# Kernel tuning notes

Hardware: AMD Instinct MI355X
Metric: run time of the kernel (lower is better)

## Reference

```python
import jax, jax.numpy as jnp
import numpy as np

N_NODES = 16   # number of per-node submodules in the DAG (topological order)
D = 2048       # per-node feature width (d_model)
B = 4096       # batch size of the in_graph tensor


def setup_inputs() -> dict:
    key = jax.random.key(0)
    kx, kw, kb = jax.random.split(key, 3)
    x = jax.random.normal(kx, (B, D), dtype=jnp.float32)
    # Per-node dense weights, scaled ~1/sqrt(D) so tanh stays in its linear-ish range
    W = jax.random.normal(kw, (N_NODES, D, D), dtype=jnp.float32) / np.float32(np.sqrt(D))
    b = jax.random.normal(kb, (N_NODES, D), dtype=jnp.float32) * np.float32(0.01)
    return {"x": x, "W": W, "b": b}


def reference(x, W, b):
    # Faithful DAG executor: iterate nodes in topological order; the address
    # book maps node i -> predecessor outputs {i-1, i-2} (node 0 reads x).
    # Each node module computes y = tanh(sum(inputs) @ W_i + b_i).
    # Loop is over the fixed structural node set (not a data dimension).
    outs = []
    for i in range(N_NODES):
        if i == 0:
            inp = x
        elif i == 1:
            inp = outs[0]
        else:
            inp = outs[i - 1] + outs[i - 2]  # address-book fan-in (sum of predecessors)
        y = jnp.tanh(inp @ W[i] + b[i])  # [B, D]
        outs.append(y)
    # _eval_forward returns the single terminal output of the DAG
    return outs[-1]
```

## Files before the change

kernel.cpp:

```cpp
#include <hip/hip_runtime.h>
#include <cstdint>
#include <cstddef>

#define NN 16
#define DD 2048
#define BB 4096

#define TM 128
#define TN 128
#define BK 64

typedef _Float16 half8 __attribute__((ext_vector_type(8)));
typedef _Float16 half4 __attribute__((ext_vector_type(4)));
typedef float f32x4 __attribute__((ext_vector_type(4)));

__device__ __forceinline__ float fast_tanh(float x) {
  float ax = __builtin_fabsf(x);
  float e = __expf(-2.0f * ax);
  float t = (1.0f - e) / (1.0f + e);
  return x < 0.0f ? -t : t;
}

__global__ __launch_bounds__(256) void wconv_kernel(const float* __restrict__ W,
                                                    _Float16* __restrict__ Wh) {
  __shared__ _Float16 tile[64][80];
  const int i = blockIdx.z;
  const int k0 = blockIdx.y * 64;
  const int n0 = blockIdx.x * 64;
  const float* Wi = W + (size_t)i * DD * DD;
  _Float16* Whi = Wh + (size_t)i * DD * DD;
  const int t = threadIdx.x;
  const int cr = t >> 4;
  const int cc = (t & 15) * 4;
#pragma unroll
  for (int p = 0; p < 4; ++p) {
    int r = p * 16 + cr;
    float4 v = *(const float4*)(Wi + (size_t)(k0 + r) * DD + n0 + cc);
    tile[cc + 0][r] = (_Float16)v.x;
    tile[cc + 1][r] = (_Float16)v.y;
    tile[cc + 2][r] = (_Float16)v.z;
    tile[cc + 3][r] = (_Float16)v.w;
  }
  __syncthreads();
  const int wr = t >> 3;
  const int wc = (t & 7) * 8;
#pragma unroll
  for (int p = 0; p < 2; ++p) {
    int n = p * 32 + wr;
    half8 v = *(const half8*)&tile[n][wc];
    *(half8*)(Whi + (size_t)(n0 + n) * DD + k0 + wc) = v;
  }
}

__global__ __launch_bounds__(256) void xconv_kernel(const float* __restrict__ x,
                                                    _Float16* __restrict__ s0) {
  size_t idx = (size_t)(blockIdx.x * 256 + threadIdx.x) * 4;
  float4 v = *(const float4*)(x + idx);
  half4 o;
  o.x = (_Float16)v.x; o.y = (_Float16)v.y; o.z = (_Float16)v.z; o.w = (_Float16)v.w;
  *(half4*)(s0 + idx) = o;
}

__global__ __launch_bounds__(256, 2) void node_gemm(
    const _Float16* __restrict__ S,
    const _Float16* __restrict__ Wt,
    const float* __restrict__ bias,
    _Float16* __restrict__ Y,
    const _Float16* __restrict__ Yprev,
    _Float16* __restrict__ Snext,
    float* __restrict__ Ofinal)
{
  __shared__ _Float16 smem[4 * TM * BK];

  const int t = threadIdx.x;
  const int lane = t & 63;
  const int wave = t >> 6;
  const int bid = blockIdx.x;
  const int n0 = (bid & 15) * TN;
  const int m0 = (bid >> 4) * TM;
  const int wm = (wave & 1) * 64;
  const int wn = (wave >> 1) * 64;
  const int lrow = lane & 15;
  const int lq = lane >> 4;

  f32x4 acc[4][4];
#pragma unroll
  for (int i = 0; i < 4; ++i)
#pragma unroll
    for (int j = 0; j < 4; ++j) acc[i][j] = (f32x4)0.0f;

  const int srow = t >> 3;
  const int ska = ((t & 7) ^ (srow & 7)) * 8;
  const _Float16* ag = S + (size_t)(m0 + srow) * DD + ska;
  const _Float16* bg = Wt + (size_t)(n0 + srow) * DD + ska;

  auto stage = [&](int p, int k0) {
    const _Float16* a = ag + k0;
    const _Float16* b = bg + k0;
    _Float16* al = smem + p * (TM * BK) + t * 8;
    _Float16* bl = smem + 2 * (TM * BK) + p * (TN * BK) + t * 8;
#pragma unroll
    for (int r = 0; r < 4; ++r) {
      __builtin_amdgcn_global_load_lds(
          (const __attribute__((address_space(1))) void*)(a + (size_t)(r * 32) * DD),
          (__attribute__((address_space(3))) void*)(al + r * 2048), 16, 0, 0);
      __builtin_amdgcn_global_load_lds(
          (const __attribute__((address_space(1))) void*)(b + (size_t)(r * 32) * DD),
          (__attribute__((address_space(3))) void*)(bl + r * 2048), 16, 0, 0);
    }
  };

  stage(0, 0);

  for (int i = 0; i < DD / BK; ++i) {
    __syncthreads();
    if (i < DD / BK - 1) stage((i + 1) & 1, (i + 1) * BK);
    const _Float16* Ap = smem + (i & 1) * (TM * BK);
    const _Float16* Bp = smem + 2 * (TM * BK) + (i & 1) * (TN * BK);
#pragma unroll
    for (int ks = 0; ks < BK; ks += 32) {
      const int cx = (((ks >> 3) + lq) ^ (lrow & 7)) * 8;
      half8 a[4], b[4];
#pragma unroll
      for (int mt = 0; mt < 4; ++mt)
        a[mt] = *(const half8*)(Ap + (wm + mt * 16 + lrow) * BK + cx);
#pragma unroll
      for (int nt = 0; nt < 4; ++nt)
        b[nt] = *(const half8*)(Bp + (wn + nt * 16 + lrow) * BK + cx);
#pragma unroll
      for (int mt = 0; mt < 4; ++mt)
#pragma unroll
        for (int nt = 0; nt < 4; ++nt)
          acc[mt][nt] =
              __builtin_amdgcn_mfma_f32_16x16x32_f16(a[mt], b[nt], acc[mt][nt], 0, 0, 0);
    }
  }

  __syncthreads();
  _Float16* CT = smem;
  float bv[4];
#pragma unroll
  for (int nt = 0; nt < 4; ++nt) bv[nt] = bias[n0 + wn + nt * 16 + lrow];
#pragma unroll
  for (int mt = 0; mt < 4; ++mt)
#pragma unroll
    for (int nt = 0; nt < 4; ++nt)
#pragma unroll
      for (int r = 0; r < 4; ++r) {
        int row = wm + mt * 16 + lq * 4 + r;
        int col = wn + nt * 16 + lrow;
        CT[row * TN + col] = (_Float16)fast_tanh(acc[mt][nt][r] + bv[nt]);
      }
  __syncthreads();

#pragma unroll
  for (int pp = 0; pp < 8; ++pp) {
    int idx = pp * 2048 + t * 8;
    int row = idx >> 7;
    int col = idx & 127;
    size_t off = (size_t)(m0 + row) * DD + n0 + col;
    half8 y = *(const half8*)&CT[idx];
    if (Ofinal) {
      float4 f0 = {(float)y[0], (float)y[1], (float)y[2], (float)y[3]};
      float4 f1 = {(float)y[4], (float)y[5], (float)y[6], (float)y[7]};
      *(float4*)(Ofinal + off) = f0;
      *(float4*)(Ofinal + off + 4) = f1;
    } else {
      *(half8*)(Y + off) = y;
      half8 s = y;
      if (Yprev) s = s + *(const half8*)(Yprev + off);
      *(half8*)(Snext + off) = s;
    }
  }
}

extern "C" void kernel_launch(void* const* d_in, const int* in_sizes, int n_in,
                              void* d_out, int out_size, void* d_ws, size_t ws_size,
                              hipStream_t stream) {
  const float* x = (const float*)d_in[0];
  const float* W = (const float*)d_in[1];
  const float* b = (const float*)d_in[2];
  float* out = (float*)d_out;
  char* ws = (char*)d_ws;

  _Float16* Wh = (_Float16*)ws;
  size_t wbytes = (size_t)NN * DD * DD * sizeof(_Float16);
  _Float16* S0 = (_Float16*)(ws + wbytes);
  _Float16* S1 = S0 + (size_t)BB * DD;
  _Float16* Y0 = S1 + (size_t)BB * DD;
  _Float16* Y1 = Y0 + (size_t)BB * DD;

  wconv_kernel<<<dim3(DD / 64, DD / 64, NN), dim3(256), 0, stream>>>(W, Wh);
  xconv_kernel<<<dim3((BB * DD) / 1024), dim3(256), 0, stream>>>(x, S0);

  _Float16* Sb[2] = {S0, S1};
  _Float16* Yb[2] = {Y0, Y1};
  dim3 ggrid((DD / TN) * (BB / TM));
  for (int i = 0; i < NN; ++i) {
    const _Float16* Sin = Sb[i & 1];
    _Float16* Sout = Sb[(i + 1) & 1];
    _Float16* Yout = Yb[i & 1];
    const _Float16* Yp = (i >= 1) ? Yb[(i + 1) & 1] : nullptr;
    const bool last = (i == NN - 1);
    node_gemm<<<ggrid, dim3(256), 0, stream>>>(Sin, Wh + (size_t)i * DD * DD,
                                               b + (size_t)i * DD, Yout, Yp, Sout,
                                               last ? out : nullptr);
  }
  (void)in_sizes; (void)n_in; (void)out_size; (void)ws_size;
}
```

Before: 1.106 ms.

## Use 256x128 tiles with 512 threads, triple-buffered LDS pipeline and XCD-aware block swizzle

Doubles the M tile to 256 and uses 8 waves per block. The LDS pipeline becomes three stages with manual vmcnt waits and barriers in place of __syncthreads, so loads stay two tiles ahead of compute. Blocks are remapped across the 8 XCDs so neighbouring tiles share cached operands, and setprio raises wave priority around the MFMA bursts. LDS use grows to about 144KB per block, which probably allows only one block per CU despite the launch bounds, and the hand-written waitcnt counts have to match the number of loads issued per stage.

```diff
diff --git a/kernel.cpp b/kernel.cpp
--- a/kernel.cpp
+++ b/kernel.cpp
@@ -6,9 +6,10 @@
 #define DD 2048
 #define BB 4096
 
-#define TM 128
+#define TM 256
 #define TN 128
 #define BK 64
+#define BUFH (TM * BK + TN * BK)
 
 typedef _Float16 half8 __attribute__((ext_vector_type(8)));
 typedef _Float16 half4 __attribute__((ext_vector_type(4)));
@@ -61,7 +62,7 @@
   *(half4*)(s0 + idx) = o;
 }
 
-__global__ __launch_bounds__(256, 2) void node_gemm(
+__global__ __launch_bounds__(512, 2) void node_gemm(
     const _Float16* __restrict__ S,
     const _Float16* __restrict__ Wt,
     const float* __restrict__ bias,
@@ -70,16 +71,17 @@
     _Float16* __restrict__ Snext,
     float* __restrict__ Ofinal)
 {
-  __shared__ _Float16 smem[4 * TM * BK];
+  __shared__ _Float16 smem[3 * BUFH];
 
   const int t = threadIdx.x;
   const int lane = t & 63;
   const int wave = t >> 6;
   const int bid = blockIdx.x;
-  const int n0 = (bid & 15) * TN;
-  const int m0 = (bid >> 4) * TM;
-  const int wm = (wave & 1) * 64;
-  const int wn = (wave >> 1) * 64;
+  const int swz = (bid & 7) * 32 + (bid >> 3);
+  const int n0 = (swz >> 4) * TN;
+  const int m0 = (swz & 15) * TM;
+  const int wm = (wave >> 1) * 64;
+  const int wn = (wave & 1) * 64;
   const int lrow = lane & 15;
   const int lq = lane >> 4;
 
@@ -94,29 +96,33 @@
   const _Float16* ag = S + (size_t)(m0 + srow) * DD + ska;
   const _Float16* bg = Wt + (size_t)(n0 + srow) * DD + ska;
 
-  auto stage = [&](int p, int k0) {
+  auto stage = [&](int buf, int k0) {
     const _Float16* a = ag + k0;
     const _Float16* b = bg + k0;
-    _Float16* al = smem + p * (TM * BK) + t * 8;
-    _Float16* bl = smem + 2 * (TM * BK) + p * (TN * BK) + t * 8;
-#pragma unroll
-    for (int r = 0; r < 4; ++r) {
+    _Float16* al = smem + buf * BUFH + t * 8;
+    _Float16* bl = smem + buf * BUFH + TM * BK + t * 8;
+#pragma unroll
+    for (int r = 0; r < 4; ++r)
       __builtin_amdgcn_global_load_lds(
-          (const __attribute__((address_space(1))) void*)(a + (size_t)(r * 32) * DD),
-          (__attribute__((address_space(3))) void*)(al + r * 2048), 16, 0, 0);
+          (const __attribute__((address_space(1))) void*)(a + (size_t)(r * 64) * DD),
+          (__attribute__((address_space(3))) void*)(al + r * 4096), 16, 0, 0);
+#pragma unroll
+    for (int r = 0; r < 2; ++r)
       __builtin_amdgcn_global_load_lds(
-          (const __attribute__((address_space(1))) void*)(b + (size_t)(r * 32) * DD),
-          (__attribute__((address_space(3))) void*)(bl + r * 2048), 16, 0, 0);
-    }
+          (const __attribute__((address_space(1))) void*)(b + (size_t)(r * 64) * DD),
+          (__attribute__((address_space(3))) void*)(bl + r * 4096), 16, 0, 0);
   };
 
   stage(0, 0);
-
+  stage(1, BK);
+  asm volatile("s_waitcnt vmcnt(6)" ::: "memory");
+  asm volatile("s_barrier" ::: "memory");
+
+  int cur = 0, nxt = 2;
   for (int i = 0; i < DD / BK; ++i) {
-    __syncthreads();
-    if (i < DD / BK - 1) stage((i + 1) & 1, (i + 1) * BK);
-    const _Float16* Ap = smem + (i & 1) * (TM * BK);
-    const _Float16* Bp = smem + 2 * (TM * BK) + (i & 1) * (TN * BK);
+    if (i <= DD / BK - 3) stage(nxt, (i + 2) * BK);
+    const _Float16* Ap = smem + cur * BUFH;
+    const _Float16* Bp = smem + cur * BUFH + TM * BK;
 #pragma unroll
     for (int ks = 0; ks < BK; ks += 32) {
       const int cx = (((ks >> 3) + lq) ^ (lrow & 7)) * 8;
@@ -127,13 +133,24 @@
 #pragma unroll
       for (int nt = 0; nt < 4; ++nt)
         b[nt] = *(const half8*)(Bp + (wn + nt * 16 + lrow) * BK + cx);
+      __builtin_amdgcn_s_setprio(1);
 #pragma unroll
       for (int mt = 0; mt < 4; ++mt)
 #pragma unroll
         for (int nt = 0; nt < 4; ++nt)
           acc[mt][nt] =
               __builtin_amdgcn_mfma_f32_16x16x32_f16(a[mt], b[nt], acc[mt][nt], 0, 0, 0);
+      __builtin_amdgcn_s_setprio(0);
     }
+    if (i < DD / BK - 2) {
+      asm volatile("s_waitcnt vmcnt(6)" ::: "memory");
+      asm volatile("s_barrier" ::: "memory");
+    } else if (i == DD / BK - 2) {
+      asm volatile("s_waitcnt vmcnt(0)" ::: "memory");
+      asm volatile("s_barrier" ::: "memory");
+    }
+    cur = (cur == 2) ? 0 : cur + 1;
+    nxt = (nxt == 2) ? 0 : nxt + 1;
   }
 
   __syncthreads();
@@ -155,7 +172,7 @@
 
 #pragma unroll
   for (int pp = 0; pp < 8; ++pp) {
-    int idx = pp * 2048 + t * 8;
+    int idx = pp * 4096 + t * 8;
     int row = idx >> 7;
     int col = idx & 127;
     size_t off = (size_t)(m0 + row) * DD + n0 + col;
@@ -195,14 +212,14 @@
 
   _Float16* Sb[2] = {S0, S1};
   _Float16* Yb[2] = {Y0, Y1};
-  dim3 ggrid((DD / TN) * (BB / TM));
+  dim3 ggrid((BB / TM) * (DD / TN));
   for (int i = 0; i < NN; ++i) {
     const _Float16* Sin = Sb[i & 1];
     _Float16* Sout = Sb[(i + 1) & 1];
     _Float16* Yout = Yb[i & 1];
     const _Float16* Yp = (i >= 1) ? Yb[(i + 1) & 1] : nullptr;
     const bool last = (i == NN - 1);
-    node_gemm<<<ggrid, dim3(256), 0, stream>>>(Sin, Wh + (size_t)i * DD * DD,
+    node_gemm<<<ggrid, dim3(512), 0, stream>>>(Sin, Wh + (size_t)i * DD * DD,
                                                b + (size_t)i * DD, Yout, Yp, Sout,
                                                last ? out : nullptr);
   }
```

Measured after the change: 1.134 ms. 2.5% more time.

## Load A operand directly to registers from MFMA-tiled layout; triple-buffer B in LDS

Applied to the files above, without the earlier changes.

The activation matrix S is now stored in a layout pre-tiled for the MFMA fragments, so each wave loads its A fragments straight from global memory into registers, one iteration ahead. Only the W tile goes through LDS, now with three buffers, two stages of lookahead and hand-placed waitcnt/barrier. The change also remaps blocks so neighbouring tiles stay on the same XCD, raises MFMA wave priority, and rewrites the weight and input conversion kernels to produce the new layout without an LDS transpose. The intent is to cut LDS traffic and stalls on barriers. In exchange there is more register pressure and fragile manual vmcnt counting.

```diff
diff --git a/kernel.cpp b/kernel.cpp
--- a/kernel.cpp
+++ b/kernel.cpp
@@ -9,10 +9,16 @@
 #define TM 128
 #define TN 128
 #define BK 64
+#define BBUF (TN * BK)
 
 typedef _Float16 half8 __attribute__((ext_vector_type(8)));
 typedef _Float16 half4 __attribute__((ext_vector_type(4)));
 typedef float f32x4 __attribute__((ext_vector_type(4)));
+
+__device__ __forceinline__ size_t tiled_off(int m, int k) {
+  return ((size_t)(m >> 4) * (DD / 32) + (k >> 5)) * 512 +
+         (size_t)(((m & 15) + ((k >> 3) & 3) * 16) * 8);
+}
 
 __device__ __forceinline__ float fast_tanh(float x) {
   float ax = __builtin_fabsf(x);
@@ -23,42 +29,45 @@
 
 __global__ __launch_bounds__(256) void wconv_kernel(const float* __restrict__ W,
                                                     _Float16* __restrict__ Wh) {
-  __shared__ _Float16 tile[64][80];
   const int i = blockIdx.z;
-  const int k0 = blockIdx.y * 64;
-  const int n0 = blockIdx.x * 64;
+  const int k0 = blockIdx.y * 128;
+  const int n0 = blockIdx.x * 128;
   const float* Wi = W + (size_t)i * DD * DD;
   _Float16* Whi = Wh + (size_t)i * DD * DD;
   const int t = threadIdx.x;
-  const int cr = t >> 4;
-  const int cc = (t & 15) * 4;
-#pragma unroll
-  for (int p = 0; p < 4; ++p) {
-    int r = p * 16 + cr;
-    float4 v = *(const float4*)(Wi + (size_t)(k0 + r) * DD + n0 + cc);
-    tile[cc + 0][r] = (_Float16)v.x;
-    tile[cc + 1][r] = (_Float16)v.y;
-    tile[cc + 2][r] = (_Float16)v.z;
-    tile[cc + 3][r] = (_Float16)v.w;
-  }
-  __syncthreads();
-  const int wr = t >> 3;
-  const int wc = (t & 7) * 8;
-#pragma unroll
-  for (int p = 0; p < 2; ++p) {
-    int n = p * 32 + wr;
-    half8 v = *(const half8*)&tile[n][wc];
-    *(half8*)(Whi + (size_t)(n0 + n) * DD + k0 + wc) = v;
+  const int kg = (t >> 4) * 8;
+  const int ng = (t & 15) * 8;
+  float4 v[8][2];
+#pragma unroll
+  for (int r = 0; r < 8; ++r) {
+    const float* p = Wi + (size_t)(k0 + kg + r) * DD + n0 + ng;
+    v[r][0] = *(const float4*)p;
+    v[r][1] = *(const float4*)(p + 4);
+  }
+#pragma unroll
+  for (int j = 0; j < 8; ++j) {
+    half8 o;
+#pragma unroll
+    for (int r = 0; r < 8; ++r) {
+      float e = (j < 4) ? ((const float*)&v[r][0])[j] : ((const float*)&v[r][1])[j - 4];
+      o[r] = (_Float16)e;
+    }
+    *(half8*)(Whi + (size_t)(n0 + ng + j) * DD + k0 + kg) = o;
   }
 }
 
 __global__ __launch_bounds__(256) void xconv_kernel(const float* __restrict__ x,
                                                     _Float16* __restrict__ s0) {
-  size_t idx = (size_t)(blockIdx.x * 256 + threadIdx.x) * 4;
-  float4 v = *(const float4*)(x + idx);
-  half4 o;
-  o.x = (_Float16)v.x; o.y = (_Float16)v.y; o.z = (_Float16)v.z; o.w = (_Float16)v.w;
-  *(half4*)(s0 + idx) = o;
+  int gid = blockIdx.x * 256 + threadIdx.x;
+  int m = gid >> 8;
+  int c8 = gid & 255;
+  const float* p = x + (size_t)m * DD + c8 * 8;
+  float4 v0 = *(const float4*)p;
+  float4 v1 = *(const float4*)(p + 4);
+  half8 o;
+  o[0] = (_Float16)v0.x; o[1] = (_Float16)v0.y; o[2] = (_Float16)v0.z; o[3] = (_Float16)v0.w;
+  o[4] = (_Float16)v1.x; o[5] = (_Float16)v1.y; o[6] = (_Float16)v1.z; o[7] = (_Float16)v1.w;
+  *(half8*)(s0 + tiled_off(m, c8 * 8)) = o;
 }
 
 __global__ __launch_bounds__(256, 2) void node_gemm(
@@ -70,16 +79,18 @@
     _Float16* __restrict__ Snext,
     float* __restrict__ Ofinal)
 {
-  __shared__ _Float16 smem[4 * TM * BK];
+  __shared__ _Float16 smem[3 * BBUF];
 
   const int t = threadIdx.x;
   const int lane = t & 63;
   const int wave = t >> 6;
   const int bid = blockIdx.x;
-  const int n0 = (bid & 15) * TN;
-  const int m0 = (bid >> 4) * TM;
-  const int wm = (wave & 1) * 64;
-  const int wn = (wave >> 1) * 64;
+  const int xcd = bid & 7;
+  const int loc = bid >> 3;
+  const int m0 = ((xcd & 3) * 8 + (loc & 7)) * TM;
+  const int n0 = ((xcd >> 2) * 8 + (loc >> 3)) * TN;
+  const int wm = (wave >> 1) * 64;
+  const int wn = (wave & 1) * 64;
   const int lrow = lane & 15;
   const int lq = lane >> 4;
 
@@ -89,51 +100,82 @@
 #pragma unroll
     for (int j = 0; j < 4; ++j) acc[i][j] = (f32x4)0.0f;
 
+  const _Float16* Ab[4];
+#pragma unroll
+  for (int mt = 0; mt < 4; ++mt)
+    Ab[mt] = S + ((size_t)((m0 + wm) >> 4) + mt) * (DD / 32) * 512 + (size_t)lane * 8;
+
   const int srow = t >> 3;
   const int ska = ((t & 7) ^ (srow & 7)) * 8;
-  const _Float16* ag = S + (size_t)(m0 + srow) * DD + ska;
   const _Float16* bg = Wt + (size_t)(n0 + srow) * DD + ska;
 
-  auto stage = [&](int p, int k0) {
-    const _Float16* a = ag + k0;
+  auto stageB = [&](int p, int k0) {
     const _Float16* b = bg + k0;
-    _Float16* al = smem + p * (TM * BK) + t * 8;
-    _Float16* bl = smem + 2 * (TM * BK) + p * (TN * BK) + t * 8;
-#pragma unroll
-    for (int r = 0; r < 4; ++r) {
-      __builtin_amdgcn_global_load_lds(
-          (const __attribute__((address_space(1))) void*)(a + (size_t)(r * 32) * DD),
-          (__attribute__((address_space(3))) void*)(al + r * 2048), 16, 0, 0);
+    _Float16* bl = smem + p * BBUF + t * 8;
+#pragma unroll
+    for (int r = 0; r < 4; ++r)
       __builtin_amdgcn_global_load_lds(
           (const __attribute__((address_space(1))) void*)(b + (size_t)(r * 32) * DD),
           (__attribute__((address_space(3))) void*)(bl + r * 2048), 16, 0, 0);
-    }
   };
 
-  stage(0, 0);
-
-  for (int i = 0; i < DD / BK; ++i) {
-    __syncthreads();
-    if (i < DD / BK - 1) stage((i + 1) & 1, (i + 1) * BK);
-    const _Float16* Ap = smem + (i & 1) * (TM * BK);
-    const _Float16* Bp = smem + 2 * (TM * BK) + (i & 1) * (TN * BK);
-#pragma unroll
-    for (int ks = 0; ks < BK; ks += 32) {
-      const int cx = (((ks >> 3) + lq) ^ (lrow & 7)) * 8;
-      half8 a[4], b[4];
+  half8 aRa[8], aRb[8];
+  int bcur = 0, bnxt = 2;
+
+#pragma unroll
+  for (int mt = 0; mt < 4; ++mt)
+#pragma unroll
+    for (int ks = 0; ks < 2; ++ks)
+      aRa[mt * 2 + ks] = *(const half8*)(Ab[mt] + (size_t)ks * 512);
+  __builtin_amdgcn_sched_barrier(0);
+  stageB(0, 0);
+  stageB(1, BK);
+  __builtin_amdgcn_sched_barrier(0);
+  asm volatile("s_waitcnt vmcnt(4)" ::: "memory");
+  asm volatile("s_barrier" ::: "memory");
+
+  auto body = [&](int i, half8(&acur)[8], half8(&anxt)[8]) {
+    if (i <= 30) {
 #pragma unroll
       for (int mt = 0; mt < 4; ++mt)
-        a[mt] = *(const half8*)(Ap + (wm + mt * 16 + lrow) * BK + cx);
+#pragma unroll
+        for (int ks = 0; ks < 2; ++ks)
+          anxt[mt * 2 + ks] =
+              *(const half8*)(Ab[mt] + (size_t)(2 * (i + 1) + ks) * 512);
+    }
+    __builtin_amdgcn_sched_barrier(0);
+    if (i <= 29) stageB(bnxt, (i + 2) * BK);
+    const _Float16* Bp = smem + bcur * BBUF;
+#pragma unroll
+    for (int ks = 0; ks < 2; ++ks) {
+      const int cx = (((ks << 2) + lq) ^ (lrow & 7)) * 8;
+      half8 b[4];
 #pragma unroll
       for (int nt = 0; nt < 4; ++nt)
         b[nt] = *(const half8*)(Bp + (wn + nt * 16 + lrow) * BK + cx);
+      __builtin_amdgcn_s_setprio(1);
 #pragma unroll
       for (int mt = 0; mt < 4; ++mt)
 #pragma unroll
         for (int nt = 0; nt < 4; ++nt)
-          acc[mt][nt] =
-              __builtin_amdgcn_mfma_f32_16x16x32_f16(a[mt], b[nt], acc[mt][nt], 0, 0, 0);
-    }
+          acc[mt][nt] = __builtin_amdgcn_mfma_f32_16x16x32_f16(
+              acur[mt * 2 + ks], b[nt], acc[mt][nt], 0, 0, 0);
+      __builtin_amdgcn_s_setprio(0);
+    }
+    if (i <= 29) {
+      asm volatile("s_waitcnt vmcnt(12)" ::: "memory");
+      asm volatile("s_barrier" ::: "memory");
+    } else if (i == 30) {
+      asm volatile("s_waitcnt vmcnt(8)" ::: "memory");
+      asm volatile("s_barrier" ::: "memory");
+    }
+    bcur = (bcur == 2) ? 0 : bcur + 1;
+    bnxt = (bnxt == 2) ? 0 : bnxt + 1;
+  };
+
+  for (int ii = 0; ii < DD / BK; ii += 2) {
+    body(ii, aRa, aRb);
+    body(ii + 1, aRb, aRa);
   }
 
   __syncthreads();
@@ -158,7 +200,9 @@
     int idx = pp * 2048 + t * 8;
     int row = idx >> 7;
     int col = idx & 127;
-    size_t off = (size_t)(m0 + row) * DD + n0 + col;
+    int gm = m0 + row;
+    int gn = n0 + col;
+    size_t off = (size_t)gm * DD + gn;
     half8 y = *(const half8*)&CT[idx];
     if (Ofinal) {
       float4 f0 = {(float)y[0], (float)y[1], (float)y[2], (float)y[3]};
@@ -169,7 +213,7 @@
       *(half8*)(Y + off) = y;
       half8 s = y;
       if (Yprev) s = s + *(const half8*)(Yprev + off);
-      *(half8*)(Snext + off) = s;
+      *(half8*)(Snext + tiled_off(gm, gn)) = s;
     }
   }
 }
@@ -190,12 +234,12 @@
   _Float16* Y0 = S1 + (size_t)BB * DD;
   _Float16* Y1 = Y0 + (size_t)BB * DD;
 
-  wconv_kernel<<<dim3(DD / 64, DD / 64, NN), dim3(256), 0, stream>>>(W, Wh);
-  xconv_kernel<<<dim3((BB * DD) / 1024), dim3(256), 0, stream>>>(x, S0);
+  wconv_kernel<<<dim3(DD / 128, DD / 128, NN), dim3(256), 0, stream>>>(W, Wh);
+  xconv_kernel<<<dim3((BB * DD) / (256 * 8)), dim3(256), 0, stream>>>(x, S0);
 
   _Float16* Sb[2] = {S0, S1};
   _Float16* Yb[2] = {Y0, Y1};
-  dim3 ggrid((DD / TN) * (BB / TM));
+  dim3 ggrid((BB / TM) * (DD / TN));
   for (int i = 0; i < NN; ++i) {
     const _Float16* Sin = Sb[i & 1];
     _Float16* Sout = Sb[(i + 1) & 1];
```

After: 1.287 ms. 16.4% more time.

## Fuse node GEMM launches into one persistent kernel with grid barrier

Applied to the files above, without the earlier changes.

Replaces the sixteen per-node GEMM launches with a single persistent kernel of 512 blocks that loops over nodes and uses an atomic-counter grid barrier between them. This removes per-launch overhead and the tail gaps between dependent kernels. It relies on all 512 blocks being co-resident (2 blocks per CU), otherwise the spin barrier can deadlock. The weight-conversion transpose kernel is also rewritten to load four rows per thread and store half4 vectors into a tighter shared tile.

```diff
diff --git a/kernel.cpp b/kernel.cpp
--- a/kernel.cpp
+++ b/kernel.cpp
@@ -9,6 +9,7 @@
 #define TM 128
 #define TN 128
 #define BK 64
+#define NBLK 512
 
 typedef _Float16 half8 __attribute__((ext_vector_type(8)));
 typedef _Float16 half4 __attribute__((ext_vector_type(4)));
@@ -23,23 +24,27 @@
 
 __global__ __launch_bounds__(256) void wconv_kernel(const float* __restrict__ W,
                                                     _Float16* __restrict__ Wh) {
-  __shared__ _Float16 tile[64][80];
+  __shared__ _Float16 tile[64][68];
   const int i = blockIdx.z;
   const int k0 = blockIdx.y * 64;
   const int n0 = blockIdx.x * 64;
   const float* Wi = W + (size_t)i * DD * DD;
   _Float16* Whi = Wh + (size_t)i * DD * DD;
   const int t = threadIdx.x;
-  const int cr = t >> 4;
-  const int cc = (t & 15) * 4;
-#pragma unroll
-  for (int p = 0; p < 4; ++p) {
-    int r = p * 16 + cr;
-    float4 v = *(const float4*)(Wi + (size_t)(k0 + r) * DD + n0 + cc);
-    tile[cc + 0][r] = (_Float16)v.x;
-    tile[cc + 1][r] = (_Float16)v.y;
-    tile[cc + 2][r] = (_Float16)v.z;
-    tile[cc + 3][r] = (_Float16)v.w;
+  const int kb = (t >> 4) * 4;
+  const int nb = (t & 15) * 4;
+  float4 v[4];
+#pragma unroll
+  for (int r = 0; r < 4; ++r)
+    v[r] = *(const float4*)(Wi + (size_t)(k0 + kb + r) * DD + n0 + nb);
+#pragma unroll
+  for (int j = 0; j < 4; ++j) {
+    half4 o;
+    o.x = (_Float16)((const float*)&v[0])[j];
+    o.y = (_Float16)((const float*)&v[1])[j];
+    o.z = (_Float16)((const float*)&v[2])[j];
+    o.w = (_Float16)((const float*)&v[3])[j];
+    *(half4*)&tile[nb + j][kb] = o;
   }
   __syncthreads();
   const int wr = t >> 3;
@@ -47,8 +52,12 @@
 #pragma unroll
   for (int p = 0; p < 2; ++p) {
     int n = p * 32 + wr;
-    half8 v = *(const half8*)&tile[n][wc];
-    *(half8*)(Whi + (size_t)(n0 + n) * DD + k0 + wc) = v;
+    half4 lo = *(const half4*)&tile[n][wc];
+    half4 hi = *(const half4*)&tile[n][wc + 4];
+    half8 y;
+    y[0] = lo.x; y[1] = lo.y; y[2] = lo.z; y[3] = lo.w;
+    y[4] = hi.x; y[5] = hi.y; y[6] = hi.z; y[7] = hi.w;
+    *(half8*)(Whi + (size_t)(n0 + n) * DD + k0 + wc) = y;
   }
 }
 
@@ -61,16 +70,42 @@
   *(half4*)(s0 + idx) = o;
 }
 
-__global__ __launch_bounds__(256, 2) void node_gemm(
-    const _Float16* __restrict__ S,
-    const _Float16* __restrict__ Wt,
-    const float* __restrict__ bias,
-    _Float16* __restrict__ Y,
-    const _Float16* __restrict__ Yprev,
-    _Float16* __restrict__ Snext,
-    float* __restrict__ Ofinal)
+__global__ void binit_kernel(unsigned* bar) {
+  if (threadIdx.x < 32) bar[threadIdx.x] = 0u;
+}
+
+__device__ __forceinline__ void grid_sync(unsigned* cnt, unsigned* gen) {
+  __syncthreads();
+  if (threadIdx.x == 0) {
+    __threadfence();
+    unsigned g = __hip_atomic_load(gen, __ATOMIC_RELAXED, __HIP_MEMORY_SCOPE_AGENT);
+    unsigned a = __hip_atomic_fetch_add(cnt, 1u, __ATOMIC_ACQ_REL, __HIP_MEMORY_SCOPE_AGENT);
+    if (a == NBLK - 1) {
+      __hip_atomic_store(cnt, 0u, __ATOMIC_RELAXED, __HIP_MEMORY_SCOPE_AGENT);
+      __hip_atomic_fetch_add(gen, 1u, __ATOMIC_RELEASE, __HIP_MEMORY_SCOPE_AGENT);
+    } else {
+      while (__hip_atomic_load(gen, __ATOMIC_ACQUIRE, __HIP_MEMORY_SCOPE_AGENT) == g)
+        __builtin_amdgcn_s_sleep(8);
+    }
+    __threadfence();
+  }
+  __syncthreads();
+}
+
+__global__ __launch_bounds__(256, 2) void node_chain(
+    const _Float16* __restrict__ Wh,
+    const float* __restrict__ bias_all,
+    _Float16* __restrict__ S0,
+    _Float16* __restrict__ S1,
+    _Float16* __restrict__ Y0,
+    _Float16* __restrict__ Y1,
+    float* __restrict__ Ofinal,
+    unsigned* __restrict__ bar)
 {
   __shared__ _Float16 smem[4 * TM * BK];
+
+  unsigned* cnt = bar;
+  unsigned* gen = bar + 16;
 
   const int t = threadIdx.x;
   const int lane = t & 63;
@@ -83,94 +118,107 @@
   const int lrow = lane & 15;
   const int lq = lane >> 4;
 
-  f32x4 acc[4][4];
-#pragma unroll
-  for (int i = 0; i < 4; ++i)
-#pragma unroll
-    for (int j = 0; j < 4; ++j) acc[i][j] = (f32x4)0.0f;
-
   const int srow = t >> 3;
   const int ska = ((t & 7) ^ (srow & 7)) * 8;
-  const _Float16* ag = S + (size_t)(m0 + srow) * DD + ska;
-  const _Float16* bg = Wt + (size_t)(n0 + srow) * DD + ska;
-
-  auto stage = [&](int p, int k0) {
-    const _Float16* a = ag + k0;
-    const _Float16* b = bg + k0;
-    _Float16* al = smem + p * (TM * BK) + t * 8;
-    _Float16* bl = smem + 2 * (TM * BK) + p * (TN * BK) + t * 8;
-#pragma unroll
-    for (int r = 0; r < 4; ++r) {
-      __builtin_amdgcn_global_load_lds(
-          (const __attribute__((address_space(1))) void*)(a + (size_t)(r * 32) * DD),
-          (__attribute__((address_space(3))) void*)(al + r * 2048), 16, 0, 0);
-      __builtin_amdgcn_global_load_lds(
-          (const __attribute__((address_space(1))) void*)(b + (size_t)(r * 32) * DD),
-          (__attribute__((address_space(3))) void*)(bl + r * 2048), 16, 0, 0);
+
+  for (int node = 0; node < NN; ++node) {
+    const _Float16* S = (node & 1) ? S1 : S0;
+    _Float16* Snext = (node & 1) ? S0 : S1;
+    _Float16* Y = (node & 1) ? Y1 : Y0;
+    const _Float16* Yprev = (node >= 1) ? ((node & 1) ? Y0 : Y1) : nullptr;
+    const _Float16* Wt = Wh + (size_t)node * DD * DD;
+    const float* bias = bias_all + (size_t)node * DD;
+    const bool last = (node == NN - 1);
+
+    f32x4 acc[4][4];
+#pragma unroll
+    for (int i = 0; i < 4; ++i)
+#pragma unroll
+      for (int j = 0; j < 4; ++j) acc[i][j] = (f32x4)0.0f;
+
+    const _Float16* ag = S + (size_t)(m0 + srow) * DD + ska;
+    const _Float16* bg = Wt + (size_t)(n0 + srow) * DD + ska;
+
+    auto stage = [&](int p, int k0) {
+      const _Float16* a = ag + k0;
+      const _Float16* b = bg + k0;
+      _Float16* al = smem + p * (TM * BK) + t * 8;
+      _Float16* bl = smem + 2 * (TM * BK) + p * (TN * BK) + t * 8;
+#pragma unroll
+      for (int r = 0; r < 4; ++r) {
+        __builtin_amdgcn_global_load_lds(
+            (const __attribute__((address_space(1))) void*)(a + (size_t)(r * 32) * DD),
+            (__attribute__((address_space(3))) void*)(al + r * 2048), 16, 0, 0);
+        __builtin_amdgcn_global_load_lds(
+            (const __attribute__((address_space(1))) void*)(b + (size_t)(r * 32) * DD),
+            (__attribute__((address_space(3))) void*)(bl + r * 2048), 16, 0, 0);
+      }
+    };
+
+    stage(0, 0);
+
+    for (int i = 0; i < DD / BK; ++i) {
+      __syncthreads();
+      if (i < DD / BK - 1) stage((i + 1) & 1, (i + 1) * BK);
+      const _Float16* Ap = smem + (i & 1) * (TM * BK);
+      const _Float16* Bp = smem + 2 * (TM * BK) + (i & 1) * (TN * BK);
+#pragma unroll
+      for (int ks = 0; ks < BK; ks += 32) {
+        const int cx = (((ks >> 3) + lq) ^ (lrow & 7)) * 8;
+        half8 a[4], b[4];
+#pragma unroll
+        for (int mt = 0; mt < 4; ++mt)
+          a[mt] = *(const half8*)(Ap + (wm + mt * 16 + lrow) * BK + cx);
+#pragma unroll
+        for (int nt = 0; nt < 4; ++nt)
+          b[nt] = *(const half8*)(Bp + (wn + nt * 16 + lrow) * BK + cx);
+#pragma unroll
+        for (int mt = 0; mt < 4; ++mt)
+#pragma unroll
+          for (int nt = 0; nt < 4; ++nt)
+            acc[mt][nt] =
+                __builtin_amdgcn_mfma_f32_16x16x32_f16(a[mt], b[nt], acc[mt][nt], 0, 0, 0);
+      }
     }
-  };
-
-  stage(0, 0);
-
-  for (int i = 0; i < DD / BK; ++i) {
+
     __syncthreads();
-    if (i < DD / BK - 1) stage((i + 1) & 1, (i + 1) * BK);
-    const _Float16* Ap = smem + (i & 1) * (TM * BK);
-    const _Float16* Bp = smem + 2 * (TM * BK) + (i & 1) * (TN * BK);
-#pragma unroll
-    for (int ks = 0; ks < BK; ks += 32) {
-      const int cx = (((ks >> 3) + lq) ^ (lrow & 7)) * 8;
-      half8 a[4], b[4];
-#pragma unroll
-      for (int mt = 0; mt < 4; ++mt)
-        a[mt] = *(const half8*)(Ap + (wm + mt * 16 + lrow) * BK + cx);
+    _Float16* CT = smem;
+    float bv[4];
+#pragma unroll
+    for (int nt = 0; nt < 4; ++nt) bv[nt] = bias[n0 + wn + nt * 16 + lrow];
+#pragma unroll
+    for (int mt = 0; mt < 4; ++mt)
 #pragma unroll
       for (int nt = 0; nt < 4; ++nt)
-        b[nt] = *(const half8*)(Bp + (wn + nt * 16 + lrow) * BK + cx);
-#pragma unroll
-      for (int mt = 0; mt < 4; ++mt)
-#pragma unroll
-        for (int nt = 0; nt < 4; ++nt)
-          acc[mt][nt] =
-              __builtin_amdgcn_mfma_f32_16x16x32_f16(a[mt], b[nt], acc[mt][nt], 0, 0, 0);
+#pragma unroll
+        for (int r = 0; r < 4; ++r) {
+          int row = wm + mt * 16 + lq * 4 + r;
+          int col = wn + nt * 16 + lrow;
+          CT[row * TN + col] = (_Float16)fast_tanh(acc[mt][nt][r] + bv[nt]);
+        }
+    __syncthreads();
+
+#pragma unroll
+    for (int pp = 0; pp < 8; ++pp) {
+      int idx = pp * 2048 + t * 8;
+      int row = idx >> 7;
+      int col = idx & 127;
+      size_t off = (size_t)(m0 + row) * DD + n0 + col;
+      half8 y = *(const half8*)&CT[idx];
+      if (last) {
+        float4 f0 = {(float)y[0], (float)y[1], (float)y[2], (float)y[3]};
+        float4 f1 = {(float)y[4], (float)y[5], (float)y[6], (float)y[7]};
+        *(float4*)(Ofinal + off) = f0;
+        *(float4*)(Ofinal + off + 4) = f1;
+      } else {
+        *(half8*)(Y + off) = y;
+        half8 s = y;
+        if (Yprev) s = s + *(const half8*)(Yprev + off);
+        *(half8*)(Snext + off) = s;
+      }
     }
-  }
-
-  __syncthreads();
-  _Float16* CT = smem;
-  float bv[4];
-#pragma unroll
-  for (int nt = 0; nt < 4; ++nt) bv[nt] = bias[n0 + wn + nt * 16 + lrow];
-#pragma unroll
-  for (int mt = 0; mt < 4; ++mt)
-#pragma unroll
-    for (int nt = 0; nt < 4; ++nt)
-#pragma unroll
-      for (int r = 0; r < 4; ++r) {
-        int row = wm + mt * 16 + lq * 4 + r;
-        int col = wn + nt * 16 + lrow;
-        CT[row * TN + col] = (_Float16)fast_tanh(acc[mt][nt][r] + bv[nt]);
-      }
-  __syncthreads();
-
-#pragma unroll
-  for (int pp = 0; pp < 8; ++pp) {
-    int idx = pp * 2048 + t * 8;
-    int row = idx >> 7;
-    int col = idx & 127;
-    size_t off = (size_t)(m0 + row) * DD + n0 + col;
-    half8 y = *(const half8*)&CT[idx];
-    if (Ofinal) {
-      float4 f0 = {(float)y[0], (float)y[1], (float)y[2], (float)y[3]};
-      float4 f1 = {(float)y[4], (float)y[5], (float)y[6], (float)y[7]};
-      *(float4*)(Ofinal + off) = f0;
-      *(float4*)(Ofinal + off + 4) = f1;
-    } else {
-      *(half8*)(Y + off) = y;
-      half8 s = y;
-      if (Yprev) s = s + *(const half8*)(Yprev + off);
-      *(half8*)(Snext + off) = s;
-    }
+
+    if (!last) grid_sync(cnt, gen);
   }
 }
 
@@ -185,26 +233,17 @@
 
   _Float16* Wh = (_Float16*)ws;
   size_t wbytes = (size_t)NN * DD * DD * sizeof(_Float16);
+  size_t sbytes = (size_t)BB * DD * sizeof(_Float16);
   _Float16* S0 = (_Float16*)(ws + wbytes);
   _Float16* S1 = S0 + (size_t)BB * DD;
   _Float16* Y0 = S1 + (size_t)BB * DD;
   _Float16* Y1 = Y0 + (size_t)BB * DD;
-
+  unsigned* bar = (unsigned*)(ws + wbytes + 4 * sbytes);
+
+  binit_kernel<<<dim3(1), dim3(64), 0, stream>>>(bar);
   wconv_kernel<<<dim3(DD / 64, DD / 64, NN), dim3(256), 0, stream>>>(W, Wh);
   xconv_kernel<<<dim3((BB * DD) / 1024), dim3(256), 0, stream>>>(x, S0);
 
-  _Float16* Sb[2] = {S0, S1};
-  _Float16* Yb[2] = {Y0, Y1};
-  dim3 ggrid((DD / TN) * (BB / TM));
-  for (int i = 0; i < NN; ++i) {
-    const _Float16* Sin = Sb[i & 1];
-    _Float16* Sout = Sb[(i + 1) & 1];
-    _Float16* Yout = Yb[i & 1];
-    const _Float16* Yp = (i >= 1) ? Yb[(i + 1) & 1] : nullptr;
-    const bool last = (i == NN - 1);
-    node_gemm<<<ggrid, dim3(256), 0, stream>>>(Sin, Wh + (size_t)i * DD * DD,
-                                               b + (size_t)i * DD, Yout, Yp, Sout,
-                                               last ? out : nullptr);
-  }
+  node_chain<<<dim3(NBLK), dim3(256), 0, stream>>>(Wh, b, S0, S1, Y0, Y1, out, bar);
   (void)in_sizes; (void)n_in; (void)out_size; (void)ws_size;
 }
```

Measured after the change: 2.559 ms. 131% more time.
